# Kernel tuning notes

Measured on AMD Instinct MI355X. Metric: run time of the kernel, lower is better.

Reference implementation:

```python
import jax, jax.numpy as jnp
import numpy as np

# Human3.6M skeleton: 16 bones over 17 joints
SKELETON = [(0,1),(1,2),(2,3),(0,4),(4,5),(5,6),(0,7),(7,8),(8,9),(9,10),(8,11),(11,12),(12,13),(8,14),(14,15),(15,16)]
PARENT = jnp.array([p for p, c in SKELETON], dtype=jnp.int32)
CHILD = jnp.array([c for p, c in SKELETON], dtype=jnp.int32)
NUM_BONES = 16
EPS = 1e-9


def setup_inputs() -> dict:
    key = jax.random.key(0)
    k1, k2, k3, k4, k5 = jax.random.split(key, 5)
    B, J = 1000000, 17
    pred_jts = jax.random.normal(k1, (B, J, 3), dtype=jnp.float32)
    gt_bl = jax.random.uniform(k2, (B, NUM_BONES), dtype=jnp.float32)
    anchor_scores = jax.random.uniform(k3, (B, J), dtype=jnp.float32)
    # ShiftAttention params: fc1 (32->16), fc2 (16->32), no bias; stored as [in, out]
    W1 = jax.random.normal(k4, (2 * NUM_BONES, NUM_BONES), dtype=jnp.float32) * (2.0 / (2 * NUM_BONES)) ** 0.5
    W2 = jax.random.normal(k5, (NUM_BONES, 2 * NUM_BONES), dtype=jnp.float32) * (2.0 / NUM_BONES) ** 0.5
    return {"pred_jts": pred_jts, "gt_bl": gt_bl, "anchor_scores": anchor_scores, "W1": W1, "W2": W2}


def reference(pred_jts, gt_bl, anchor_scores, W1, W2):
    B = pred_jts.shape[0]
    # per-edge gather: bone vectors [B, 16, 3]
    diff = pred_jts[:, PARENT, :] - pred_jts[:, CHILD, :]
    bl_norm = jnp.linalg.norm(diff, axis=-1)            # [B, 16]
    dis_bl = gt_bl - bl_norm                            # bone-length error
    a_p = anchor_scores[:, PARENT]
    a_c = anchor_scores[:, CHILD]
    a_sum = a_p + a_c + EPS
    # split correction between parent (weighted by child score) and child
    move_bl = jnp.stack([dis_bl * a_c / a_sum, dis_bl * a_p / a_sum], axis=-1)  # [B, 16, 2]
    # ShiftAttention gate: sigmoid(relu(x W1) W2)
    x = move_bl.reshape(B, 2 * NUM_BONES)
    gate = jax.nn.sigmoid(jax.nn.relu(x @ W1) @ W2).reshape(B, NUM_BONES, 2)
    move_bl = move_bl * gate
    # unit bone directions and per-edge forces
    unit = diff / (bl_norm[..., None] + EPS)            # [B, 16, 3]
    force_parent = move_bl[..., 0:1] * unit
    force_child = -move_bl[..., 1:2] * unit
    # scatter-add forces into joints (duplicate joint indices accumulate)
    move_jts = jnp.zeros_like(pred_jts).at[:, PARENT].add(force_parent).at[:, CHILD].add(force_child)
    return pred_jts + move_jts
```

## Files before the change

### kernel.cpp

```cpp
#include <hip/hip_runtime.h>

#define DEV __device__ __forceinline__

#define LDS_FENCE() asm volatile("s_waitcnt lgkmcnt(0)" ::: "memory")
#define VM_FENCE()  asm volatile("s_waitcnt vmcnt(0)" ::: "memory")

DEV void gload_lds16(const void* g, void* lds) {
    __builtin_amdgcn_global_load_lds(
        (const __attribute__((address_space(1))) void*)g,
        (__attribute__((address_space(3))) void*)lds,
        16, 0, 0);
}

DEV float4 fma4(float4 acc, float s, float4 v) {
    acc.x = fmaf(s, v.x, acc.x);
    acc.y = fmaf(s, v.y, acc.y);
    acc.z = fmaf(s, v.z, acc.z);
    acc.w = fmaf(s, v.w, acc.w);
    return acc;
}

DEV float fast_sigmoid(float v) {
    return __builtin_amdgcn_rcpf(1.0f + __builtin_amdgcn_exp2f(-1.4426950408889634f * v));
}

DEV void compute_sample(const float (&p)[51], const float (&a)[17], const float (&g)[16],
                        const float* sW1, const float* sW2, float (&o)[51])
{
    constexpr int PAR[16] = {0,1,2,0,4,5,0,7,8,9,8,11,12,8,14,15};
    constexpr int CHI[16] = {1,2,3,4,5,6,7,8,9,10,11,12,13,14,15,16};

    float x[32], invn[16];
    #pragma unroll
    for (int k = 0; k < 16; ++k) {
        const int P = PAR[k] * 3, C = CHI[k] * 3;
        const float dx = p[P]   - p[C];
        const float dy = p[P+1] - p[C+1];
        const float dz = p[P+2] - p[C+2];
        const float n  = __builtin_amdgcn_sqrtf(fmaf(dx,dx, fmaf(dy,dy, dz*dz)));
        const float dis = g[k] - n;
        const float ap = a[PAR[k]], ac = a[CHI[k]];
        const float inv_asum = __builtin_amdgcn_rcpf(ap + ac + 1e-9f);
        x[2*k]   = dis * ac * inv_asum;
        x[2*k+1] = dis * ap * inv_asum;
        invn[k]  = __builtin_amdgcn_rcpf(n + 1e-9f);
    }

    const float4* w1v = reinterpret_cast<const float4*>(sW1);
    const float4* w2v = reinterpret_cast<const float4*>(sW2);

    float4 y0 = {0,0,0,0}, y1 = {0,0,0,0}, y2 = {0,0,0,0}, y3 = {0,0,0,0};
    #pragma unroll
    for (int i = 0; i < 32; ++i) {
        const float xi = x[i];
        y0 = fma4(y0, xi, w1v[i*4+0]);
        y1 = fma4(y1, xi, w1v[i*4+1]);
        y2 = fma4(y2, xi, w1v[i*4+2]);
        y3 = fma4(y3, xi, w1v[i*4+3]);
    }
    float h[16];
    h[0]=fmaxf(y0.x,0.f);  h[1]=fmaxf(y0.y,0.f);  h[2]=fmaxf(y0.z,0.f);  h[3]=fmaxf(y0.w,0.f);
    h[4]=fmaxf(y1.x,0.f);  h[5]=fmaxf(y1.y,0.f);  h[6]=fmaxf(y1.z,0.f);  h[7]=fmaxf(y1.w,0.f);
    h[8]=fmaxf(y2.x,0.f);  h[9]=fmaxf(y2.y,0.f);  h[10]=fmaxf(y2.z,0.f); h[11]=fmaxf(y2.w,0.f);
    h[12]=fmaxf(y3.x,0.f); h[13]=fmaxf(y3.y,0.f); h[14]=fmaxf(y3.z,0.f); h[15]=fmaxf(y3.w,0.f);

    float xg[32];
    #pragma unroll
    for (int c = 0; c < 8; ++c) {
        float4 gq = {0,0,0,0};
        #pragma unroll
        for (int j = 0; j < 16; ++j) gq = fma4(gq, h[j], w2v[j*8 + c]);
        xg[4*c+0] = x[4*c+0] * fast_sigmoid(gq.x);
        xg[4*c+1] = x[4*c+1] * fast_sigmoid(gq.y);
        xg[4*c+2] = x[4*c+2] * fast_sigmoid(gq.z);
        xg[4*c+3] = x[4*c+3] * fast_sigmoid(gq.w);
    }
    #pragma unroll
    for (int k = 0; k < 16; ++k) {
        xg[2*k]   *= invn[k];
        xg[2*k+1] *= invn[k];
    }

    #pragma unroll
    for (int j = 0; j < 17; ++j) {
        float ox = p[3*j], oy = p[3*j+1], oz = p[3*j+2];
        #pragma unroll
        for (int k = 0; k < 16; ++k) {
            if (PAR[k] == j || CHI[k] == j) {
                const int P = PAR[k] * 3, C = CHI[k] * 3;
                const float dx = p[P]   - p[C];
                const float dy = p[P+1] - p[C+1];
                const float dz = p[P+2] - p[C+2];
                const float s = (PAR[k] == j) ? xg[2*k] : -xg[2*k+1];
                ox = fmaf(s, dx, ox);
                oy = fmaf(s, dy, oy);
                oz = fmaf(s, dz, oz);
            }
        }
        o[3*j]   = ox;
        o[3*j+1] = oy;
        o[3*j+2] = oz;
    }
}

__global__ __launch_bounds__(256, 2) void projts_kernel(
    const float* __restrict__ pred,
    const float* __restrict__ gt,
    const float* __restrict__ anc,
    const float* __restrict__ gW1,
    const float* __restrict__ gW2,
    float* __restrict__ out,
    int B)
{
    constexpr int ROW = 51;
    constexpr int WBUF = 64 * ROW;
    constexpr int ABUF = 64 * 17;

    __shared__ float sW1[512]  __attribute__((aligned(16)));
    __shared__ float sW2[512]  __attribute__((aligned(16)));
    __shared__ float sbuf[4][WBUF] __attribute__((aligned(16)));
    __shared__ float abuf[4][ABUF] __attribute__((aligned(16)));

    const int t = threadIdx.x;
    {
        float4* s1 = reinterpret_cast<float4*>(sW1);
        float4* s2 = reinterpret_cast<float4*>(sW2);
        const float4* g1 = reinterpret_cast<const float4*>(gW1);
        const float4* g2 = reinterpret_cast<const float4*>(gW2);
        if (t < 128)      s1[t] = g1[t];
        else if (t < 256) s2[t - 128] = g2[t - 128];
    }
    __syncthreads();

    const int w = t >> 6;
    const int l = t & 63;
    const long long wavebase = ((long long)blockIdx.x * 4 + w) * 64;
    if (wavebase >= B) return;

    float* buf  = sbuf[w];
    float4* buf4 = reinterpret_cast<float4*>(buf);
    float* abf  = abuf[w];

    if (wavebase + 64 <= (long long)B) {
        float p[51], a[17], o[51];

        const char* srcB = reinterpret_cast<const char*>(pred + (size_t)wavebase * ROW);
        const char* ascB = reinterpret_cast<const char*>(anc + (size_t)wavebase * 17);
        char* bufB = reinterpret_cast<char*>(buf);
        char* abfB = reinterpret_cast<char*>(abf);

        #pragma unroll
        for (int i = 0; i < 12; ++i)
            gload_lds16(srcB + (size_t)(i*64 + l)*16, bufB + i*1024);
        if (l < 48)
            gload_lds16(srcB + (size_t)(768 + l)*16, bufB + 12*1024);

        #pragma unroll
        for (int i = 0; i < 4; ++i)
            gload_lds16(ascB + (size_t)(i*64 + l)*16, abfB + i*1024);
        if (l < 16)
            gload_lds16(ascB + (size_t)(256 + l)*16, abfB + 4*1024);

        const float4* gsrc4 = reinterpret_cast<const float4*>(gt + (size_t)(wavebase + l) * 16);
        const float4 gq0 = gsrc4[0], gq1 = gsrc4[1], gq2 = gsrc4[2], gq3 = gsrc4[3];

        VM_FENCE();

        #pragma unroll
        for (int j = 0; j < ROW; ++j) p[j] = buf[l*ROW + j];
        #pragma unroll
        for (int j = 0; j < 17; ++j) a[j] = abf[l*17 + j];
        LDS_FENCE();

        const float g[16] = {gq0.x,gq0.y,gq0.z,gq0.w, gq1.x,gq1.y,gq1.z,gq1.w,
                             gq2.x,gq2.y,gq2.z,gq2.w, gq3.x,gq3.y,gq3.z,gq3.w};

        compute_sample(p, a, g, sW1, sW2, o);

        #pragma unroll
        for (int j = 0; j < ROW; ++j) buf[l*ROW + j] = o[j];
        LDS_FENCE();

        float4* dst4 = reinterpret_cast<float4*>(out + (size_t)wavebase * ROW);
        #pragma unroll
        for (int i = 0; i < 12; ++i) dst4[i*64 + l] = buf4[i*64 + l];
        if (l < 48) dst4[768 + l] = buf4[768 + l];
    } else {
        const long long b = wavebase + l;
        if (b < B) {
            float p[51], a[17], g[16], o[51];
            const float* pj = pred + (size_t)b * 51;
            #pragma unroll
            for (int j = 0; j < 51; ++j) p[j] = pj[j];
            const float* ab = anc + (size_t)b * 17;
            #pragma unroll
            for (int j = 0; j < 17; ++j) a[j] = ab[j];
            const float* gb = gt + (size_t)b * 16;
            #pragma unroll
            for (int j = 0; j < 16; ++j) g[j] = gb[j];

            compute_sample(p, a, g, sW1, sW2, o);

            float* ob = out + (size_t)b * 51;
            #pragma unroll
            for (int j = 0; j < 51; ++j) ob[j] = o[j];
        }
    }
}

extern "C" void kernel_launch(void* const* d_in, const int* in_sizes, int n_in,
                              void* d_out, int out_size, void* d_ws, size_t ws_size,
                              hipStream_t stream) {
    const float* pred = (const float*)d_in[0];
    const float* gt   = (const float*)d_in[1];
    const float* anc  = (const float*)d_in[2];
    const float* W1   = (const float*)d_in[3];
    const float* W2   = (const float*)d_in[4];
    float* out = (float*)d_out;

    const int B = in_sizes[0] / 51;
    const int blocks = (B + 255) / 256;
    hipLaunchKernelGGL(projts_kernel, dim3(blocks), dim3(256), 0, stream,
                       pred, gt, anc, W1, W2, out, B);
}
```

Before: 109.5 us.

## Use packed FMA with scalar-register weights and drop LDS weight staging

The two small MLP layers are rewritten to use v_pk_fma_f32, with weight pairs fed as SGPR operands loaded straight from global memory through uniform scalar loads. The LDS copy of W1/W2 and the block-wide __syncthreads are removed. This is meant to halve the VALU FMA count and remove LDS weight reads and a barrier. The cost is a large number of scalar loads and SGPR pressure (1024 weight floats), and it relies on the compiler keeping the weights uniform so the "s" inline-asm constraint can be satisfied.

```diff
diff --git a/kernel.cpp b/kernel.cpp
--- a/kernel.cpp
+++ b/kernel.cpp
@@ -4,6 +4,8 @@
 
 #define LDS_FENCE() asm volatile("s_waitcnt lgkmcnt(0)" ::: "memory")
 #define VM_FENCE()  asm volatile("s_waitcnt vmcnt(0)" ::: "memory")
+
+typedef float f32x2 __attribute__((ext_vector_type(2)));
 
 DEV void gload_lds16(const void* g, void* lds) {
     __builtin_amdgcn_global_load_lds(
@@ -12,12 +14,8 @@
         16, 0, 0);
 }
 
-DEV float4 fma4(float4 acc, float s, float4 v) {
-    acc.x = fmaf(s, v.x, acc.x);
-    acc.y = fmaf(s, v.y, acc.y);
-    acc.z = fmaf(s, v.z, acc.z);
-    acc.w = fmaf(s, v.w, acc.w);
-    return acc;
+DEV void pk_fma_sw(f32x2& acc, f32x2 ab, f32x2 w) {
+    asm("v_pk_fma_f32 %0, %1, %2, %0" : "+v"(acc) : "v"(ab), "s"(w));
 }
 
 DEV float fast_sigmoid(float v) {
@@ -25,7 +23,8 @@
 }
 
 DEV void compute_sample(const float (&p)[51], const float (&a)[17], const float (&g)[16],
-                        const float* sW1, const float* sW2, float (&o)[51])
+                        const float* __restrict__ gW1, const float* __restrict__ gW2,
+                        float (&o)[51])
 {
     constexpr int PAR[16] = {0,1,2,0,4,5,0,7,8,9,8,11,12,8,14,15};
     constexpr int CHI[16] = {1,2,3,4,5,6,7,8,9,10,11,12,13,14,15,16};
@@ -46,34 +45,42 @@
         invn[k]  = __builtin_amdgcn_rcpf(n + 1e-9f);
     }
 
-    const float4* w1v = reinterpret_cast<const float4*>(sW1);
-    const float4* w2v = reinterpret_cast<const float4*>(sW2);
-
-    float4 y0 = {0,0,0,0}, y1 = {0,0,0,0}, y2 = {0,0,0,0}, y3 = {0,0,0,0};
+    const f32x2* W1p = reinterpret_cast<const f32x2*>(gW1);
+    const f32x2* W2p = reinterpret_cast<const f32x2*>(gW2);
+
+    f32x2 acc1[8];
+    #pragma unroll
+    for (int jj = 0; jj < 8; ++jj) acc1[jj] = (f32x2){0.f, 0.f};
     #pragma unroll
     for (int i = 0; i < 32; ++i) {
-        const float xi = x[i];
-        y0 = fma4(y0, xi, w1v[i*4+0]);
-        y1 = fma4(y1, xi, w1v[i*4+1]);
-        y2 = fma4(y2, xi, w1v[i*4+2]);
-        y3 = fma4(y3, xi, w1v[i*4+3]);
+        const f32x2 xx = {x[i], x[i]};
+        #pragma unroll
+        for (int jj = 0; jj < 8; ++jj)
+            pk_fma_sw(acc1[jj], xx, W1p[i*8 + jj]);
     }
     float h[16];
-    h[0]=fmaxf(y0.x,0.f);  h[1]=fmaxf(y0.y,0.f);  h[2]=fmaxf(y0.z,0.f);  h[3]=fmaxf(y0.w,0.f);
-    h[4]=fmaxf(y1.x,0.f);  h[5]=fmaxf(y1.y,0.f);  h[6]=fmaxf(y1.z,0.f);  h[7]=fmaxf(y1.w,0.f);
-    h[8]=fmaxf(y2.x,0.f);  h[9]=fmaxf(y2.y,0.f);  h[10]=fmaxf(y2.z,0.f); h[11]=fmaxf(y2.w,0.f);
-    h[12]=fmaxf(y3.x,0.f); h[13]=fmaxf(y3.y,0.f); h[14]=fmaxf(y3.z,0.f); h[15]=fmaxf(y3.w,0.f);
+    #pragma unroll
+    for (int jj = 0; jj < 8; ++jj) {
+        h[2*jj]   = fmaxf(acc1[jj].x, 0.f);
+        h[2*jj+1] = fmaxf(acc1[jj].y, 0.f);
+    }
+
+    f32x2 acc2[16];
+    #pragma unroll
+    for (int cc = 0; cc < 16; ++cc) acc2[cc] = (f32x2){0.f, 0.f};
+    #pragma unroll
+    for (int j = 0; j < 16; ++j) {
+        const f32x2 hh = {h[j], h[j]};
+        #pragma unroll
+        for (int cc = 0; cc < 16; ++cc)
+            pk_fma_sw(acc2[cc], hh, W2p[j*16 + cc]);
+    }
 
     float xg[32];
     #pragma unroll
-    for (int c = 0; c < 8; ++c) {
-        float4 gq = {0,0,0,0};
-        #pragma unroll
-        for (int j = 0; j < 16; ++j) gq = fma4(gq, h[j], w2v[j*8 + c]);
-        xg[4*c+0] = x[4*c+0] * fast_sigmoid(gq.x);
-        xg[4*c+1] = x[4*c+1] * fast_sigmoid(gq.y);
-        xg[4*c+2] = x[4*c+2] * fast_sigmoid(gq.z);
-        xg[4*c+3] = x[4*c+3] * fast_sigmoid(gq.w);
+    for (int cc = 0; cc < 16; ++cc) {
+        xg[2*cc]   = x[2*cc]   * fast_sigmoid(acc2[cc].x);
+        xg[2*cc+1] = x[2*cc+1] * fast_sigmoid(acc2[cc].y);
     }
     #pragma unroll
     for (int k = 0; k < 16; ++k) {
@@ -116,22 +123,10 @@
     constexpr int WBUF = 64 * ROW;
     constexpr int ABUF = 64 * 17;
 
-    __shared__ float sW1[512]  __attribute__((aligned(16)));
-    __shared__ float sW2[512]  __attribute__((aligned(16)));
     __shared__ float sbuf[4][WBUF] __attribute__((aligned(16)));
     __shared__ float abuf[4][ABUF] __attribute__((aligned(16)));
 
     const int t = threadIdx.x;
-    {
-        float4* s1 = reinterpret_cast<float4*>(sW1);
-        float4* s2 = reinterpret_cast<float4*>(sW2);
-        const float4* g1 = reinterpret_cast<const float4*>(gW1);
-        const float4* g2 = reinterpret_cast<const float4*>(gW2);
-        if (t < 128)      s1[t] = g1[t];
-        else if (t < 256) s2[t - 128] = g2[t - 128];
-    }
-    __syncthreads();
-
     const int w = t >> 6;
     const int l = t & 63;
     const long long wavebase = ((long long)blockIdx.x * 4 + w) * 64;
@@ -175,7 +170,7 @@
         const float g[16] = {gq0.x,gq0.y,gq0.z,gq0.w, gq1.x,gq1.y,gq1.z,gq1.w,
                              gq2.x,gq2.y,gq2.z,gq2.w, gq3.x,gq3.y,gq3.z,gq3.w};
 
-        compute_sample(p, a, g, sW1, sW2, o);
+        compute_sample(p, a, g, gW1, gW2, o);
 
         #pragma unroll
         for (int j = 0; j < ROW; ++j) buf[l*ROW + j] = o[j];
@@ -199,7 +194,7 @@
             #pragma unroll
             for (int j = 0; j < 16; ++j) g[j] = gb[j];
 
-            compute_sample(p, a, g, sW1, sW2, o);
+            compute_sample(p, a, g, gW1, gW2, o);
 
             float* ob = out + (size_t)b * 51;
             #pragma unroll
```

Result: slower. 136.5 us (+24.7%).
